# Kernel optimization log

Measured on AMD Instinct MI355X. Metric: run time of the kernel, lower is better.

Reference implementation:

```python
import jax, jax.numpy as jnp
import numpy as np

LOSS_WEIGHT = 1.0


def _pairwise_l1(x, y):
    # x: [B, N, 3], y: [B, M, 3] -> d: [B, N, M] with d[b,i,j] = sum_k |x[b,i,k]-y[b,j,k]|
    # Loop over the fixed D=3 coordinate axis to avoid a [B,N,M,3] intermediate.
    d = jnp.abs(x[:, :, None, 0] - y[:, None, :, 0])
    for k in range(1, x.shape[-1]):
        d = d + jnp.abs(x[:, :, None, k] - y[:, None, :, k])
    return d


def setup_inputs() -> dict:
    key = jax.random.key(0)
    kx, ky = jax.random.split(key)
    mesh_x = jax.random.normal(kx, (4, 4096, 3), dtype=jnp.float32)
    mesh_y = jax.random.normal(ky, (4, 4096, 3), dtype=jnp.float32)
    return {"mesh_x": mesh_x, "mesh_y": mesh_y}


def reference(mesh_x, mesh_y):
    # pytorch3d chamfer_distance(norm=1), point_reduction='mean', batch_reduction='mean'
    d = _pairwise_l1(mesh_x, mesh_y)          # [B, N, M]
    cham_x = jnp.min(d, axis=2)               # [B, N] nearest y for each x
    cham_y = jnp.min(d, axis=1)               # [B, M] nearest x for each y
    # mean over points then mean over batch == global mean (uniform N, M)
    loss = jnp.mean(cham_x) + jnp.mean(cham_y)
    return LOSS_WEIGHT * loss
```

## Files before the change

kernel.cpp:

```cpp
#include <hip/hip_runtime.h>

#define BATCH 4
#define NPTS  4096
#define TPB   256
#define PPT   8
#define PB    (TPB * PPT)
#define QC    64
#define ZMAX  64

__device__ __forceinline__ void min3(float& m, float a, float b) {
    asm("v_min3_f32 %0, %0, %1, %2" : "+v"(m) : "v"(a), "v"(b));
}

__global__ __launch_bounds__(TPB) void chamfer_all(const float* __restrict__ X,
                                                   const float* __restrict__ Y,
                                                   float* __restrict__ pmin,
                                                   float* __restrict__ out,
                                                   int zsteps) {
    if (blockIdx.x == 0 && blockIdx.y == 0 && blockIdx.z == 0 && threadIdx.x == 0)
        out[0] = 0.0f;

    const int dir = blockIdx.y >> 2;
    const int b   = blockIdx.y & 3;
    const int z   = blockIdx.z;
    const float* __restrict__ P = dir ? Y : X;
    const float* __restrict__ Q = dir ? X : Y;

    float px[PPT], py[PPT], pz[PPT], m[PPT];
    const int i0 = blockIdx.x * PB + threadIdx.x;
    #pragma unroll
    for (int u = 0; u < PPT; ++u) {
        const float* Pp = P + ((size_t)b * NPTS + i0 + u * TPB) * 3;
        px[u] = Pp[0];
        py[u] = Pp[1];
        pz[u] = Pp[2];
        m[u]  = __builtin_inff();
    }

    __shared__ float4 sq[QC];
    const int q0 = z * zsteps * QC;

    for (int s = 0; s < zsteps; ++s) {
        __syncthreads();
        const float* __restrict__ Qb = Q + ((size_t)b * NPTS + q0 + s * QC) * 3;
        for (int k = threadIdx.x; k < QC; k += TPB)
            sq[k] = make_float4(Qb[3 * k], Qb[3 * k + 1], Qb[3 * k + 2], 0.0f);
        __syncthreads();

        #pragma unroll 4
        for (int j = 0; j < QC; j += 2) {
            const float4 qa = sq[j];
            const float4 qb = sq[j + 1];
            #pragma unroll
            for (int u = 0; u < PPT; ++u) {
                float d0 = fabsf(px[u] - qa.x) + fabsf(py[u] - qa.y) + fabsf(pz[u] - qa.z);
                float d1 = fabsf(px[u] - qb.x) + fabsf(py[u] - qb.y) + fabsf(pz[u] - qb.z);
                min3(m[u], d0, d1);
            }
        }
    }

    float* dst = pmin + ((size_t)dir * gridDim.z + z) * (BATCH * NPTS) + b * NPTS + i0;
    #pragma unroll
    for (int u = 0; u < PPT; ++u) dst[u * TPB] = m[u];
}

__global__ __launch_bounds__(256) void reduce_loss(const float* __restrict__ pmin,
                                                   float* __restrict__ out, int Z) {
    const int half = BATCH * NPTS;
    const int s    = blockIdx.x * 256 + threadIdx.x;
    const int dir  = s >> 14;
    const int idx  = s & (half - 1);

    const float* __restrict__ base = pmin + (size_t)dir * Z * half + idx;
    float v = base[0];
    for (int z = 1; z < Z; ++z) v = fminf(v, base[(size_t)z * half]);

    for (int off = 32; off > 0; off >>= 1) v += __shfl_down(v, off, 64);

    __shared__ float partial[4];
    if ((threadIdx.x & 63) == 0) partial[threadIdx.x >> 6] = v;
    __syncthreads();
    if (threadIdx.x == 0) {
        float t = (partial[0] + partial[1] + partial[2] + partial[3]) *
                  (1.0f / (float)half);
        atomicAdd(out, t);
    }
}

extern "C" void kernel_launch(void* const* d_in, const int* in_sizes, int n_in,
                              void* d_out, int out_size, void* d_ws, size_t ws_size,
                              hipStream_t stream) {
    const float* X = (const float*)d_in[0];
    const float* Y = (const float*)d_in[1];
    float* out = (float*)d_out;
    float* pmin = (float*)d_ws;

    int Z = ZMAX;
    while (Z > 1 && (size_t)2 * Z * BATCH * NPTS * sizeof(float) > ws_size) Z >>= 1;
    const int zsteps = ZMAX / Z;

    dim3 grid(NPTS / PB, 2 * BATCH, Z);
    chamfer_all<<<grid, TPB, 0, stream>>>(X, Y, pmin, out, zsteps);

    reduce_loss<<<(2 * BATCH * NPTS) / 256, 256, 0, stream>>>(pmin, out, Z);
}
```

Before: 85.43 us.

## Vectorize point loads/stores, prefetch first Q chunk, use abs-modifier adds

Each thread now owns eight contiguous points, loaded as six float4 reads and written back with two float4 stores instead of strided scalar accesses. The first query chunk is loaded into registers before the point loads and stored to shared memory without a leading barrier. The L1 distance uses inline v_add_f32 with absolute-value source modifiers so the abs costs no separate instructions. The risks are worse coalescing across the wavefront, since each thread now touches a contiguous 96-byte span, and inline asm that can restrict compiler scheduling.

```diff
diff --git a/kernel.cpp b/kernel.cpp
--- a/kernel.cpp
+++ b/kernel.cpp
@@ -10,6 +10,17 @@
 
 __device__ __forceinline__ void min3(float& m, float a, float b) {
     asm("v_min3_f32 %0, %0, %1, %2" : "+v"(m) : "v"(a), "v"(b));
+}
+
+__device__ __forceinline__ float add_abs2(float a, float b) {
+    float d;
+    asm("v_add_f32 %0, |%1|, |%2|" : "=v"(d) : "v"(a), "v"(b));
+    return d;
+}
+__device__ __forceinline__ float add_abs1(float acc, float c) {
+    float d;
+    asm("v_add_f32 %0, %1, |%2|" : "=v"(d) : "v"(acc), "v"(c));
+    return d;
 }
 
 __global__ __launch_bounds__(TPB) void chamfer_all(const float* __restrict__ X,
@@ -26,25 +37,45 @@
     const float* __restrict__ P = dir ? Y : X;
     const float* __restrict__ Q = dir ? X : Y;
 
-    float px[PPT], py[PPT], pz[PPT], m[PPT];
-    const int i0 = blockIdx.x * PB + threadIdx.x;
-    #pragma unroll
-    for (int u = 0; u < PPT; ++u) {
-        const float* Pp = P + ((size_t)b * NPTS + i0 + u * TPB) * 3;
-        px[u] = Pp[0];
-        py[u] = Pp[1];
-        pz[u] = Pp[2];
-        m[u]  = __builtin_inff();
-    }
-
     __shared__ float4 sq[QC];
     const int q0 = z * zsteps * QC;
 
+    float s0x = 0.f, s0y = 0.f, s0z = 0.f;
+    {
+        const float* __restrict__ Qb = Q + ((size_t)b * NPTS + q0) * 3;
+        if (threadIdx.x < QC) {
+            s0x = Qb[3 * threadIdx.x];
+            s0y = Qb[3 * threadIdx.x + 1];
+            s0z = Qb[3 * threadIdx.x + 2];
+        }
+    }
+
+    const int i0 = (blockIdx.x * TPB + threadIdx.x) * PPT;
+    const float4* __restrict__ Psrc =
+        (const float4*)(P + ((size_t)b * NPTS + i0) * 3);
+    const float4 v0 = Psrc[0], v1 = Psrc[1], v2 = Psrc[2];
+    const float4 v3 = Psrc[3], v4 = Psrc[4], v5 = Psrc[5];
+
+    float px[PPT], py[PPT], pz[PPT], m[PPT];
+    px[0]=v0.x; py[0]=v0.y; pz[0]=v0.z;  px[1]=v0.w; py[1]=v1.x; pz[1]=v1.y;
+    px[2]=v1.z; py[2]=v1.w; pz[2]=v2.x;  px[3]=v2.y; py[3]=v2.z; pz[3]=v2.w;
+    px[4]=v3.x; py[4]=v3.y; pz[4]=v3.z;  px[5]=v3.w; py[5]=v4.x; pz[5]=v4.y;
+    px[6]=v4.z; py[6]=v4.w; pz[6]=v5.x;  px[7]=v5.y; py[7]=v5.z; pz[7]=v5.w;
+    #pragma unroll
+    for (int u = 0; u < PPT; ++u) m[u] = __builtin_inff();
+
     for (int s = 0; s < zsteps; ++s) {
-        __syncthreads();
-        const float* __restrict__ Qb = Q + ((size_t)b * NPTS + q0 + s * QC) * 3;
-        for (int k = threadIdx.x; k < QC; k += TPB)
-            sq[k] = make_float4(Qb[3 * k], Qb[3 * k + 1], Qb[3 * k + 2], 0.0f);
+        if (s == 0) {
+            if (threadIdx.x < QC) sq[threadIdx.x] = make_float4(s0x, s0y, s0z, 0.f);
+        } else {
+            __syncthreads();
+            const float* __restrict__ Qb =
+                Q + ((size_t)b * NPTS + q0 + s * QC) * 3;
+            if (threadIdx.x < QC)
+                sq[threadIdx.x] = make_float4(Qb[3 * threadIdx.x],
+                                              Qb[3 * threadIdx.x + 1],
+                                              Qb[3 * threadIdx.x + 2], 0.f);
+        }
         __syncthreads();
 
         #pragma unroll 4
@@ -53,16 +84,19 @@
             const float4 qb = sq[j + 1];
             #pragma unroll
             for (int u = 0; u < PPT; ++u) {
-                float d0 = fabsf(px[u] - qa.x) + fabsf(py[u] - qa.y) + fabsf(pz[u] - qa.z);
-                float d1 = fabsf(px[u] - qb.x) + fabsf(py[u] - qb.y) + fabsf(pz[u] - qb.z);
+                float a0 = px[u] - qa.x, a1 = py[u] - qa.y, a2 = pz[u] - qa.z;
+                float b0 = px[u] - qb.x, b1 = py[u] - qb.y, b2 = pz[u] - qb.z;
+                float d0 = add_abs1(add_abs2(a0, a1), a2);
+                float d1 = add_abs1(add_abs2(b0, b1), b2);
                 min3(m[u], d0, d1);
             }
         }
     }
 
-    float* dst = pmin + ((size_t)dir * gridDim.z + z) * (BATCH * NPTS) + b * NPTS + i0;
-    #pragma unroll
-    for (int u = 0; u < PPT; ++u) dst[u * TPB] = m[u];
+    float* dst = pmin + ((size_t)dir * gridDim.z + z) * (BATCH * NPTS) +
+                 b * NPTS + i0;
+    *(float4*)dst       = make_float4(m[0], m[1], m[2], m[3]);
+    *((float4*)dst + 1) = make_float4(m[4], m[5], m[6], m[7]);
 }
 
 __global__ __launch_bounds__(256) void reduce_loss(const float* __restrict__ pmin,
```

Result: faster. 82.76 us (-3.1%).
